# Optimization experiments

Hardware: AMD Instinct MI355X
Metric: run time of the kernel (lower is better)

Reference implementation:

```python
import jax, jax.numpy as jnp
import numpy as np

D = 2048
M = 50000
B = 16384
TOP_K = 5


def setup_inputs() -> dict:
    key = jax.random.key(0)
    ks = jax.random.split(key, 10)
    s = 0.02  # weight init scale
    return {
        "neural_output": jax.random.normal(ks[0], (B, D), dtype=jnp.float32),
        "context_embedding": jax.random.normal(ks[1], (D,), dtype=jnp.float32),
        "memory_bank": jax.random.normal(ks[2], (M, D), dtype=jnp.float32),
        "memory_values": jax.random.normal(ks[3], (M, D), dtype=jnp.float32),
        "Wq": jax.random.normal(ks[4], (D, D), dtype=jnp.float32) * s,
        "bq": jnp.zeros((D,), dtype=jnp.float32),
        "Wk": jax.random.normal(ks[5], (D, D), dtype=jnp.float32) * s,
        "bk": jnp.zeros((D,), dtype=jnp.float32),
        "Wv": jax.random.normal(ks[6], (D, D), dtype=jnp.float32) * s,
        "bv": jnp.zeros((D,), dtype=jnp.float32),
        "Wg": jax.random.normal(ks[7], (D, 2 * D), dtype=jnp.float32) * s,
        "bg": jnp.zeros((D,), dtype=jnp.float32),
        "top_k": TOP_K,
    }


def reference(neural_output, context_embedding, memory_bank, memory_values,
              Wq, bq, Wk, bk, Wv, bv, Wg, bg, top_k):
    d = neural_output.shape[-1]
    eps = 1e-12  # F.normalize eps

    # --- retrieve_memories: cosine similarity + top-k over the full (all-used) bank ---
    q_norm = context_embedding / jnp.maximum(jnp.linalg.norm(context_embedding), eps)
    keys_norm = memory_bank / jnp.maximum(
        jnp.linalg.norm(memory_bank, axis=-1, keepdims=True), eps)
    sims = keys_norm @ q_norm                      # [M]
    top_sims, top_idx = jax.lax.top_k(sims, top_k)  # [K], [K]
    memories = memory_values[top_idx]               # [K, D]

    # --- modulate_neural_activity: tiny cross-attention + gate ---
    q = neural_output @ Wq.T + bq                   # [B, D]
    k = memories @ Wk.T + bk                        # [K, D]
    v = memories @ Wv.T + bv                        # [K, D]
    scores = (q @ k.T) / jnp.sqrt(jnp.float32(d))   # [B, K]
    scores = scores * top_sims[None, :]             # similarity-weighted logits
    attn = jax.nn.softmax(scores, axis=-1)          # [B, K]
    attended = attn @ v                             # [B, D]

    combined = jnp.concatenate([neural_output, attended], axis=-1)  # [B, 2D]
    gate = jax.nn.sigmoid(combined @ Wg.T + bg)     # [B, D]
    return neural_output + gate * attended
```

## Files before the change

### kernel.cpp

```cpp
#include <hip/hip_runtime.h>
#include <hip/hip_bf16.h>
#include <math.h>

#define D 2048
#define M_ROWS 50000
#define B_ROWS 16384
#define TOPK 5
#define EPSN 1e-12f

typedef __attribute__((ext_vector_type(4))) float f32x4;
typedef __attribute__((ext_vector_type(8))) short s16x8;
typedef __attribute__((ext_vector_type(4))) unsigned short u16x4;

__device__ __forceinline__ unsigned short f2bf(float f) {
  union { float f; unsigned int u; } x; x.f = f;
  unsigned int u = x.u;
  unsigned int r = u + 0x7fffu + ((u >> 16) & 1u);
  return (unsigned short)(r >> 16);
}

__device__ __forceinline__ void gload16(const void* g, void* l) {
  __builtin_amdgcn_global_load_lds(
      (const __attribute__((address_space(1))) unsigned int*)g,
      (__attribute__((address_space(3))) unsigned int*)l, 16, 0, 0);
}

__global__ void k_qnorm(const float* __restrict__ ce, float* __restrict__ qn) {
  __shared__ float red[256];
  int tid = threadIdx.x;
  float s = 0.f;
  for (int t = tid; t < D; t += 256) { float x = ce[t]; s += x * x; }
  red[tid] = s; __syncthreads();
  for (int w = 128; w > 0; w >>= 1) { if (tid < w) red[tid] += red[tid + w]; __syncthreads(); }
  float inv = 1.0f / fmaxf(sqrtf(red[0]), EPSN);
  for (int t = tid; t < D; t += 256) qn[t] = ce[t] * inv;
}

__global__ void k_sims(const float* __restrict__ bank, const float* __restrict__ qn,
                       float* __restrict__ sims) {
  __shared__ float qs[D];
  int tid = threadIdx.x;
  for (int t = tid; t < D; t += 256) qs[t] = qn[t];
  __syncthreads();
  int lane = tid & 63, wid = tid >> 6;
  int gw = (blockIdx.x << 2) + wid;
  int nw = gridDim.x << 2;
  for (int m = gw; m < M_ROWS; m += nw) {
    const float* row = bank + (size_t)m * D;
    float dot = 0.f, sq = 0.f;
#pragma unroll
    for (int i = 0; i < 8; ++i) {
      int off = i * 256 + lane * 4;
      f32x4 a = *(const f32x4*)(row + off);
      f32x4 q = *(const f32x4*)(qs + off);
      dot += a[0]*q[0] + a[1]*q[1] + a[2]*q[2] + a[3]*q[3];
      sq  += a[0]*a[0] + a[1]*a[1] + a[2]*a[2] + a[3]*a[3];
    }
    for (int off = 32; off; off >>= 1) {
      dot += __shfl_xor(dot, off, 64);
      sq  += __shfl_xor(sq,  off, 64);
    }
    if (lane == 0) sims[m] = dot / fmaxf(sqrtf(sq), EPSN);
  }
}

__global__ void k_topk(const float* __restrict__ sims, float* __restrict__ top_sims,
                       int* __restrict__ top_idx) {
  __shared__ float sval[256 * TOPK];
  __shared__ int   sidx[256 * TOPK];
  __shared__ float sv2[64 * TOPK];
  __shared__ int   si2[64 * TOPK];
  int tid = threadIdx.x;
  float lv[TOPK]; int li[TOPK];
#pragma unroll
  for (int j = 0; j < TOPK; ++j) { lv[j] = -INFINITY; li[j] = 0x7fffffff; }
  for (int m = tid; m < M_ROWS; m += 256) {
    float v = sims[m];
    if (v > lv[TOPK-1] || (v == lv[TOPK-1] && m < li[TOPK-1])) {
      lv[TOPK-1] = v; li[TOPK-1] = m;
#pragma unroll
      for (int j = TOPK-1; j > 0; --j) {
        bool sw = (lv[j] > lv[j-1]) || (lv[j] == lv[j-1] && li[j] < li[j-1]);
        if (sw) { float tv=lv[j]; lv[j]=lv[j-1]; lv[j-1]=tv; int ti=li[j]; li[j]=li[j-1]; li[j-1]=ti; }
      }
    }
  }
#pragma unroll
  for (int j = 0; j < TOPK; ++j) { sval[tid*TOPK+j] = lv[j]; sidx[tid*TOPK+j] = li[j]; }
  __syncthreads();
  if (tid < 64) {
    float bv[TOPK]; int bi[TOPK];
    for (int j = 0; j < TOPK; ++j) { bv[j] = -INFINITY; bi[j] = 0x7fffffff; }
    for (int c = tid * 20; c < tid * 20 + 20; ++c) {
      float v = sval[c]; int i = sidx[c];
      if (v > bv[TOPK-1] || (v == bv[TOPK-1] && i < bi[TOPK-1])) {
        bv[TOPK-1] = v; bi[TOPK-1] = i;
        for (int j = TOPK-1; j > 0; --j) {
          bool sw = (bv[j] > bv[j-1]) || (bv[j] == bv[j-1] && bi[j] < bi[j-1]);
          if (sw) { float tv=bv[j]; bv[j]=bv[j-1]; bv[j-1]=tv; int ti=bi[j]; bi[j]=bi[j-1]; bi[j-1]=ti; }
        }
      }
    }
    for (int j = 0; j < TOPK; ++j) { sv2[tid*TOPK+j] = bv[j]; si2[tid*TOPK+j] = bi[j]; }
  }
  __syncthreads();
  if (tid == 0) {
    float bvv[TOPK]; int bii[TOPK];
    for (int j = 0; j < TOPK; ++j) { bvv[j] = -INFINITY; bii[j] = 0x7fffffff; }
    for (int c = 0; c < 64 * TOPK; ++c) {
      float v = sv2[c]; int i = si2[c];
      if (v > bvv[TOPK-1] || (v == bvv[TOPK-1] && i < bii[TOPK-1])) {
        bvv[TOPK-1] = v; bii[TOPK-1] = i;
        for (int j = TOPK-1; j > 0; --j) {
          bool sw = (bvv[j] > bvv[j-1]) || (bvv[j] == bvv[j-1] && bii[j] < bii[j-1]);
          if (sw) { float tv=bvv[j]; bvv[j]=bvv[j-1]; bvv[j-1]=tv; int ti=bii[j]; bii[j]=bii[j-1]; bii[j-1]=ti; }
        }
      }
    }
    for (int j = 0; j < TOPK; ++j) { top_sims[j] = bvv[j]; top_idx[j] = bii[j]; }
  }
}

__global__ void k_kv(const float* __restrict__ mvals, const int* __restrict__ top_idx,
                     const float* __restrict__ Wk, const float* __restrict__ bk,
                     const float* __restrict__ Wv, const float* __restrict__ bvp,
                     float* __restrict__ kb, float* __restrict__ vb) {
  __shared__ float mem[TOPK][D];
  int tid = threadIdx.x;
  for (int j = 0; j < TOPK; ++j) {
    const float* src = mvals + (size_t)top_idx[j] * D;
    for (int t = tid; t < D; t += 256) mem[j][t] = src[t];
  }
  __syncthreads();
  int lane = tid & 63, wid = tid >> 6;
  int c = blockIdx.x * 4 + wid;
  const float* wkr = Wk + (size_t)c * D;
  const float* wvr = Wv + (size_t)c * D;
  float ak[TOPK] = {0,0,0,0,0}, av[TOPK] = {0,0,0,0,0};
#pragma unroll 2
  for (int i = 0; i < 8; ++i) {
    int off = i * 256 + lane * 4;
    f32x4 wk4 = *(const f32x4*)(wkr + off);
    f32x4 wv4 = *(const f32x4*)(wvr + off);
#pragma unroll
    for (int j = 0; j < TOPK; ++j) {
      f32x4 mv = *(const f32x4*)(&mem[j][off]);
      ak[j] += mv[0]*wk4[0] + mv[1]*wk4[1] + mv[2]*wk4[2] + mv[3]*wk4[3];
      av[j] += mv[0]*wv4[0] + mv[1]*wv4[1] + mv[2]*wv4[2] + mv[3]*wv4[3];
    }
  }
  for (int off = 32; off; off >>= 1) {
#pragma unroll
    for (int j = 0; j < TOPK; ++j) {
      ak[j] += __shfl_xor(ak[j], off, 64);
      av[j] += __shfl_xor(av[j], off, 64);
    }
  }
  if (lane == 0) {
#pragma unroll
    for (int j = 0; j < TOPK; ++j) { kb[j*D + c] = ak[j] + bk[c]; vb[j*D + c] = av[j] + bvp[c]; }
  }
}

__global__ void k_prep(const float* __restrict__ Wq, const float* __restrict__ bq,
                       const float* __restrict__ Wg,
                       const float* __restrict__ kb, const float* __restrict__ vb,
                       float* __restrict__ KQpart, float* __restrict__ VW,
                       float* __restrict__ sbias, unsigned short* __restrict__ B_sw) {
  __shared__ float sh[TOPK * D];
  int tid = threadIdx.x;
  int bid = blockIdx.x;
  if (bid < 256) {
    int cc = bid >> 3, tc = bid & 7;
    for (int x = tid; x < TOPK * 64; x += 256) sh[x] = kb[(x >> 6) * D + cc * 64 + (x & 63)];
    __syncthreads();
    float acc[TOPK] = {0,0,0,0,0};
    const float* wq = Wq + (size_t)(cc * 64) * D + tc * 256 + tid;
#pragma unroll 4
    for (int c = 0; c < 64; ++c) {
      float w = wq[(size_t)c * D];
#pragma unroll
      for (int j = 0; j < TOPK; ++j) acc[j] += sh[j * 64 + c] * w;
    }
#pragma unroll
    for (int j = 0; j < TOPK; ++j)
      KQpart[(size_t)(cc * TOPK + j) * D + tc * 256 + tid] = acc[j];
  } else if (bid < 768) {
    for (int x = tid; x < TOPK * D; x += 256) sh[x] = vb[x];
    __syncthreads();
    int lane = tid & 63, wid = tid >> 6;
    int c = (bid - 256) * 4 + wid;
    const float* wg = Wg + (size_t)c * (2 * D) + D;
    float acc[TOPK] = {0,0,0,0,0};
#pragma unroll 2
    for (int i = 0; i < 8; ++i) {
      int off = i * 256 + lane * 4;
      f32x4 g4 = *(const f32x4*)(wg + off);
#pragma unroll
      for (int j = 0; j < TOPK; ++j) {
        f32x4 vv = *(const f32x4*)(&sh[j*D + off]);
        acc[j] += vv[0]*g4[0] + vv[1]*g4[1] + vv[2]*g4[2] + vv[3]*g4[3];
      }
    }
    for (int off = 32; off; off >>= 1)
#pragma unroll
      for (int j = 0; j < TOPK; ++j) acc[j] += __shfl_xor(acc[j], off, 64);
    if (lane == 0)
      for (int j = 0; j < TOPK; ++j) VW[j*D + c] = acc[j];
  } else if (bid == 768) {
    for (int j = 0; j < TOPK; ++j) {
      float s = 0.f;
      for (int t = tid; t < D; t += 256) s += bq[t] * kb[j*D + t];
      sh[tid] = s; __syncthreads();
      for (int w = 128; w > 0; w >>= 1) { if (tid < w) sh[tid] += sh[tid + w]; __syncthreads(); }
      if (tid == 0) sbias[j] = sh[0];
      __syncthreads();
    }
  } else {
    int base = (bid - 769) * 1024;
#pragma unroll
    for (int it = 0; it < 4; ++it) {
      int id = base + it * 256 + tid;
      int r = id >> 8;
      int cidx = id & 255;
      int kb_ = cidx >> 3, c = cidx & 7;
      const float* src = Wg + (size_t)r * (2 * D) + kb_ * 64 + c * 8;
      f32x4 a = *(const f32x4*)(src);
      f32x4 b = *(const f32x4*)(src + 4);
      s16x8 p;
      p[0]=(short)f2bf(a[0]); p[1]=(short)f2bf(a[1]); p[2]=(short)f2bf(a[2]); p[3]=(short)f2bf(a[3]);
      p[4]=(short)f2bf(b[0]); p[5]=(short)f2bf(b[1]); p[6]=(short)f2bf(b[2]); p[7]=(short)f2bf(b[3]);
      int dst = kb_ * 64 + ((c ^ (r & 7)) * 8);
      *(s16x8*)(B_sw + (size_t)r * D + dst) = p;
    }
  }
}

__global__ void k_red(const float* __restrict__ KQpart, float* __restrict__ KQ) {
  int x = blockIdx.x * 256 + threadIdx.x;
  float s = 0.f;
#pragma unroll 8
  for (int cc = 0; cc < 32; ++cc) s += KQpart[(size_t)cc * (TOPK * D) + x];
  KQ[x] = s;
}

template <bool WRITE_CAST>
__global__ void k_attn(const float* __restrict__ no, const float* __restrict__ KQ,
                       const float* __restrict__ sbias, const float* __restrict__ top_sims,
                       float* __restrict__ attn, unsigned short* __restrict__ A_sw) {
  __shared__ float kq[TOPK * D];
  int tid = threadIdx.x;
  for (int x = tid; x < TOPK * D; x += 256) kq[x] = KQ[x];
  __syncthreads();
  int lane = tid & 63, wid = tid >> 6;
  int gw = blockIdx.x * 4 + wid, nw = gridDim.x * 4;
  const float inv = 0.02209708691207961f;
  for (int b = gw; b < B_ROWS; b += nw) {
    const float* row = no + (size_t)b * D;
    float acc[TOPK] = {0,0,0,0,0};
    int swz = (b & 7) << 4;
#pragma unroll 2
    for (int i = 0; i < 8; ++i) {
      int off = i * 256 + lane * 4;
      f32x4 n4 = *(const f32x4*)(row + off);
#pragma unroll
      for (int j = 0; j < TOPK; ++j) {
        f32x4 kv = *(const f32x4*)(&kq[j*D + off]);
        acc[j] += n4[0]*kv[0] + n4[1]*kv[1] + n4[2]*kv[2] + n4[3]*kv[3];
      }
      if (WRITE_CAST) {
        u16x4 c4;
        c4[0]=f2bf(n4[0]); c4[1]=f2bf(n4[1]); c4[2]=f2bf(n4[2]); c4[3]=f2bf(n4[3]);
        int bytecol = off * 2;
        *(u16x4*)((char*)A_sw + (size_t)b * (D*2) + (bytecol ^ swz)) = c4;
      }
    }
    for (int off = 32; off; off >>= 1)
#pragma unroll
      for (int j = 0; j < TOPK; ++j) acc[j] += __shfl_xor(acc[j], off, 64);
    if (lane == 0) {
      float s[TOPK], mx = -INFINITY;
      for (int j = 0; j < TOPK; ++j) { s[j] = (acc[j] + sbias[j]) * inv * top_sims[j]; mx = fmaxf(mx, s[j]); }
      float sum = 0.f;
      for (int j = 0; j < TOPK; ++j) { s[j] = __expf(s[j] - mx); sum += s[j]; }
      float r = 1.0f / sum;
      for (int j = 0; j < TOPK; ++j) attn[(size_t)b*TOPK + j] = s[j] * r;
    }
  }
}

union GemmSmem {
  struct { unsigned short A[2][256 * 64]; unsigned short B[2][256 * 64]; } s;
  float ep[4096];
};

__global__ __launch_bounds__(512, 2) void k_gemm_bf(
    const unsigned short* __restrict__ A_sw, const unsigned short* __restrict__ B_sw,
    const float* __restrict__ no, const float* __restrict__ bg,
    const float* __restrict__ attn, const float* __restrict__ vb,
    const float* __restrict__ VW, float* __restrict__ out) {
  __shared__ GemmSmem sm;

  int tid = threadIdx.x;
  int lane = tid & 63, wid = tid >> 6;
  int fr = lane & 15, fg = lane >> 4;
  int wr = wid >> 2, wc = wid & 3;

  int id = blockIdx.x;
  int nt = id & 7, mt = id >> 3;
  int brow = mt * 256, bcol = nt * 256;

  f32x4 acc[8][4];
#pragma unroll
  for (int m = 0; m < 8; ++m)
#pragma unroll
    for (int n = 0; n < 4; ++n) acc[m][n] = (f32x4){0.f, 0.f, 0.f, 0.f};

  const unsigned short* gA[4];
  const unsigned short* gB[4];
  int lofs[4];
#pragma unroll
  for (int i = 0; i < 4; ++i) {
    int cid = i * 512 + tid;
    int row = cid >> 3, cc = cid & 7;
    gA[i] = A_sw + (size_t)(brow + row) * D + cc * 8;
    gB[i] = B_sw + (size_t)(bcol + row) * D + cc * 8;
    lofs[i] = (i * 512 + wid * 64) * 8;
  }

#pragma unroll
  for (int i = 0; i < 4; ++i) {
    gload16(gA[i], sm.s.A[0] + lofs[i]);
    gload16(gB[i], sm.s.B[0] + lofs[i]);
  }
#pragma unroll
  for (int i = 0; i < 4; ++i) { gA[i] += 64; gB[i] += 64; }
  __syncthreads();

  int cur = 0;
  for (int kt = 0; kt < 32; ++kt) {
    if (kt < 31) {
#pragma unroll
      for (int i = 0; i < 4; ++i) {
        gload16(gA[i], sm.s.A[cur ^ 1] + lofs[i]);
        gload16(gB[i], sm.s.B[cur ^ 1] + lofs[i]);
      }
#pragma unroll
      for (int i = 0; i < 4; ++i) { gA[i] += 64; gB[i] += 64; }
    }
    const unsigned short* Ab = sm.s.A[cur];
    const unsigned short* Bb = sm.s.B[cur];
#pragma unroll
    for (int kk = 0; kk < 2; ++kk) {
      s16x8 af[8], bfr[4];
#pragma unroll
      for (int m = 0; m < 8; ++m) {
        int row = wr * 128 + m * 16 + fr;
        int addr = row * 128 + ((kk * 64 + fg * 16) ^ ((row & 7) << 4));
        af[m] = *(const s16x8*)((const char*)Ab + addr);
      }
#pragma unroll
      for (int n = 0; n < 4; ++n) {
        int row = wc * 64 + n * 16 + fr;
        int addr = row * 128 + ((kk * 64 + fg * 16) ^ ((row & 7) << 4));
        bfr[n] = *(const s16x8*)((const char*)Bb + addr);
      }
#pragma unroll
      for (int m = 0; m < 8; ++m)
#pragma unroll
        for (int n = 0; n < 4; ++n)
          acc[m][n] = __builtin_amdgcn_mfma_f32_16x16x32_bf16(af[m], bfr[n], acc[m][n], 0, 0, 0);
    }
    __syncthreads();
    cur ^= 1;
  }

  for (int x = tid; x < 1280; x += 512) sm.ep[x] = attn[(size_t)brow * TOPK + x];
  for (int x = tid; x < 1280; x += 512) { int j = x >> 8, c = x & 255; sm.ep[1280 + x] = VW[j*D + bcol + c]; }
  for (int x = tid; x < 1280; x += 512) { int j = x >> 8, c = x & 255; sm.ep[2560 + x] = vb[j*D + bcol + c]; }
  if (tid < 256) sm.ep[3840 + tid] = bg[bcol + tid];
  __syncthreads();

#pragma unroll
  for (int m = 0; m < 8; ++m) {
    int rbase = wr * 128 + m * 16 + fg * 4;
#pragma unroll
    for (int n = 0; n < 4; ++n) {
      int c = wc * 64 + n * 16 + fr;
      float vw0 = sm.ep[1280 + 0*256 + c], vw1 = sm.ep[1280 + 1*256 + c], vw2 = sm.ep[1280 + 2*256 + c],
            vw3 = sm.ep[1280 + 3*256 + c], vw4 = sm.ep[1280 + 4*256 + c];
      float v0 = sm.ep[2560 + 0*256 + c], v1 = sm.ep[2560 + 1*256 + c], v2 = sm.ep[2560 + 2*256 + c],
            v3 = sm.ep[2560 + 3*256 + c], v4 = sm.ep[2560 + 4*256 + c];
      float bgc = sm.ep[3840 + c];
#pragma unroll
      for (int i = 0; i < 4; ++i) {
        int r = rbase + i;
        float a0 = sm.ep[r*5+0], a1 = sm.ep[r*5+1], a2 = sm.ep[r*5+2], a3 = sm.ep[r*5+3], a4 = sm.ep[r*5+4];
        float gl = acc[m][n][i] + bgc + a0*vw0 + a1*vw1 + a2*vw2 + a3*vw3 + a4*vw4;
        float att = a0*v0 + a1*v1 + a2*v2 + a3*v3 + a4*v4;
        float gate = 1.0f / (1.0f + __expf(-gl));
        size_t gi = (size_t)(brow + r) * D + bcol + c;
        out[gi] = no[gi] + gate * att;
      }
    }
  }
}

#define BM 128
#define BN 128
#define BKf 32
#define LDK (BKf + 8)

__global__ __launch_bounds__(256) void k_gemm_f32(
    const float* __restrict__ no, const float* __restrict__ Wg,
    const float* __restrict__ bg, const float* __restrict__ attn,
    const float* __restrict__ vb, const float* __restrict__ VW,
    float* __restrict__ out) {
  __shared__ unsigned short As[BM * LDK];
  __shared__ unsigned short Bs[BN * LDK];
  __shared__ float ep[2048];

  int tid = threadIdx.x;
  int lane = tid & 63, wid = tid >> 6;
  int brow = blockIdx.x * BM;
  int bcol = blockIdx.y * BN;
  int wr = wid >> 1, wc = wid & 1;

  f32x4 acc[4][4];
#pragma unroll
  for (int m = 0; m < 4; ++m)
#pragma unroll
    for (int n = 0; n < 4; ++n) acc[m][n] = (f32x4){0.f, 0.f, 0.f, 0.f};

  int fr = lane & 15, fg = lane >> 4;

  for (int kt = 0; kt < D / BKf; ++kt) {
    int k0 = kt * BKf;
#pragma unroll
    for (int i = 0; i < 4; ++i) {
      int fid = tid + i * 256;
      int row = fid >> 3, c4 = (fid & 7) * 4;
      f32x4 a4 = *(const f32x4*)(no + (size_t)(brow + row) * D + k0 + c4);
      f32x4 b4 = *(const f32x4*)(Wg + (size_t)(bcol + row) * (2 * D) + k0 + c4);
      u16x4 ab, bb;
      ab[0] = f2bf(a4[0]); ab[1] = f2bf(a4[1]); ab[2] = f2bf(a4[2]); ab[3] = f2bf(a4[3]);
      bb[0] = f2bf(b4[0]); bb[1] = f2bf(b4[1]); bb[2] = f2bf(b4[2]); bb[3] = f2bf(b4[3]);
      *(u16x4*)(&As[row * LDK + c4]) = ab;
      *(u16x4*)(&Bs[row * LDK + c4]) = bb;
    }
    __syncthreads();
    s16x8 af[4], bfr[4];
#pragma unroll
    for (int m = 0; m < 4; ++m) af[m] = *(const s16x8*)(&As[(wr*64 + m*16 + fr) * LDK + fg*8]);
#pragma unroll
    for (int n = 0; n < 4; ++n) bfr[n] = *(const s16x8*)(&Bs[(wc*64 + n*16 + fr) * LDK + fg*8]);
#pragma unroll
    for (int m = 0; m < 4; ++m)
#pragma unroll
      for (int n = 0; n < 4; ++n)
        acc[m][n] = __builtin_amdgcn_mfma_f32_16x16x32_bf16(af[m], bfr[n], acc[m][n], 0, 0, 0);
    __syncthreads();
  }

  for (int x = tid; x < 640; x += 256) ep[x] = attn[(size_t)brow * TOPK + x];
  for (int x = tid; x < 640; x += 256) { int j = x >> 7, c = x & 127; ep[640 + x]  = VW[j*D + bcol + c]; }
  for (int x = tid; x < 640; x += 256) { int j = x >> 7, c = x & 127; ep[1280 + x] = vb[j*D + bcol + c]; }
  if (tid < 128) ep[1920 + tid] = bg[bcol + tid];
  __syncthreads();

#pragma unroll
  for (int m = 0; m < 4; ++m) {
    int rbase = wr * 64 + m * 16 + fg * 4;
#pragma unroll
    for (int n = 0; n < 4; ++n) {
      int c = wc * 64 + n * 16 + fr;
      float vw0 = ep[640 + 0*128 + c], vw1 = ep[640 + 1*128 + c], vw2 = ep[640 + 2*128 + c],
            vw3 = ep[640 + 3*128 + c], vw4 = ep[640 + 4*128 + c];
      float v0 = ep[1280 + 0*128 + c], v1 = ep[1280 + 1*128 + c], v2 = ep[1280 + 2*128 + c],
            v3 = ep[1280 + 3*128 + c], v4 = ep[1280 + 4*128 + c];
      float bgc = ep[1920 + c];
#pragma unroll
      for (int i = 0; i < 4; ++i) {
        int r = rbase + i;
        float a0 = ep[r*5+0], a1 = ep[r*5+1], a2 = ep[r*5+2], a3 = ep[r*5+3], a4 = ep[r*5+4];
        float gl = acc[m][n][i] + bgc + a0*vw0 + a1*vw1 + a2*vw2 + a3*vw3 + a4*vw4;
        float att = a0*v0 + a1*v1 + a2*v2 + a3*v3 + a4*v4;
        float gate = 1.0f / (1.0f + __expf(-gl));
        size_t gi = (size_t)(brow + r) * D + bcol + c;
        out[gi] = no[gi] + gate * att;
      }
    }
  }
}

extern "C" void kernel_launch(void* const* d_in, const int* in_sizes, int n_in,
                              void* d_out, int out_size, void* d_ws, size_t ws_size,
                              hipStream_t stream) {
  (void)in_sizes; (void)n_in; (void)out_size;
  const float* no    = (const float*)d_in[0];
  const float* ce    = (const float*)d_in[1];
  const float* bank  = (const float*)d_in[2];
  const float* mvals = (const float*)d_in[3];
  const float* Wq    = (const float*)d_in[4];
  const float* bq    = (const float*)d_in[5];
  const float* Wk    = (const float*)d_in[6];
  const float* bk    = (const float*)d_in[7];
  const float* Wv    = (const float*)d_in[8];
  const float* bvp   = (const float*)d_in[9];
  const float* Wg    = (const float*)d_in[10];
  const float* bg    = (const float*)d_in[11];
  float* out = (float*)d_out;

  char* ws = (char*)d_ws;
  float* qn       = (float*)(ws + 0);
  float* sims     = (float*)(ws + 16384);
  float* top_sims = (float*)(ws + 220160);
  int*   top_idx  = (int*)  (ws + 220192);
  float* sbias    = (float*)(ws + 220224);
  float* kb       = (float*)(ws + 221184);
  float* vb       = (float*)(ws + 262144);
  float* VW       = (float*)(ws + 303104);
  float* KQpart   = (float*)(ws + 344064);
  float* KQ       = (float*)(ws + 1654784);
  float* attn     = (float*)(ws + 1695744);
  unsigned short* A_sw = (unsigned short*)(ws + 4194304);
  unsigned short* B_sw = (unsigned short*)(ws + 4194304 + (size_t)B_ROWS * D * 2);

  const size_t ws_need = 4194304 + (size_t)B_ROWS * D * 2 + (size_t)D * D * 2;
  const bool fast = ws_size >= ws_need;

  k_qnorm<<<1, 256, 0, stream>>>(ce, qn);
  k_sims<<<1024, 256, 0, stream>>>(bank, qn, sims);
  k_topk<<<1, 256, 0, stream>>>(sims, top_sims, top_idx);
  k_kv<<<512, 256, 0, stream>>>(mvals, top_idx, Wk, bk, Wv, bvp, kb, vb);
  k_prep<<<fast ? 1281 : 769, 256, 0, stream>>>(Wq, bq, Wg, kb, vb, KQpart, VW, sbias, B_sw);
  k_red<<<40, 256, 0, stream>>>(KQpart, KQ);
  if (fast) {
    k_attn<true><<<1024, 256, 0, stream>>>(no, KQ, sbias, top_sims, attn, A_sw);
    k_gemm_bf<<<512, 512, 0, stream>>>(A_sw, B_sw, no, bg, attn, vb, VW, out);
  } else {
    k_attn<false><<<1024, 256, 0, stream>>>(no, KQ, sbias, top_sims, attn, A_sw);
    k_gemm_f32<<<dim3(B_ROWS / BM, D / BN), 256, 0, stream>>>(no, Wg, bg, attn, vb, VW, out);
  }
}
```

Baseline: 562.0 us.

## Pre-tile GEMM operands into MFMA subtiles and interleave loads with MFMA phases

The bf16 cast kernels now write A and B into a 16-row by 64-column subtile layout, so each wave's global-to-LDS copy is one contiguous 1 KB chunk and fragment reads need no XOR swizzle. The GEMM main loop is split into four phases that alternate LDS fragment reads, staging of the next k-tile's halves, and MFMA bursts. These phases use raw s_barrier, explicit waitcnt and setprio so that memory traffic overlaps with compute. Launch bounds drop to one block per SIMD set, which relies on intra-block overlap instead of occupancy and brings a risk of LDS race or stall issues from the hand-tuned waitcnt counts.

```diff
diff --git a/kernel.cpp b/kernel.cpp
--- a/kernel.cpp
+++ b/kernel.cpp
@@ -23,6 +23,11 @@
   __builtin_amdgcn_global_load_lds(
       (const __attribute__((address_space(1))) unsigned int*)g,
       (__attribute__((address_space(3))) unsigned int*)l, 16, 0, 0);
+}
+
+__device__ __forceinline__ size_t sub_addr(int row, int k) {
+  return ((size_t)(row >> 4) * 32 + (size_t)(k >> 6)) * 1024
+       + (size_t)(((k >> 5) & 1) * 512 + ((k >> 3) & 3) * 128 + (row & 15) * 8);
 }
 
 __global__ void k_qnorm(const float* __restrict__ ce, float* __restrict__ qn) {
@@ -220,18 +225,16 @@
     int base = (bid - 769) * 1024;
 #pragma unroll
     for (int it = 0; it < 4; ++it) {
-      int id = base + it * 256 + tid;
-      int r = id >> 8;
-      int cidx = id & 255;
-      int kb_ = cidx >> 3, c = cidx & 7;
-      const float* src = Wg + (size_t)r * (2 * D) + kb_ * 64 + c * 8;
+      int id2 = base + it * 256 + tid;
+      int r = id2 >> 8;
+      int k = (id2 & 255) * 8;
+      const float* src = Wg + (size_t)r * (2 * D) + k;
       f32x4 a = *(const f32x4*)(src);
       f32x4 b = *(const f32x4*)(src + 4);
       s16x8 p;
       p[0]=(short)f2bf(a[0]); p[1]=(short)f2bf(a[1]); p[2]=(short)f2bf(a[2]); p[3]=(short)f2bf(a[3]);
       p[4]=(short)f2bf(b[0]); p[5]=(short)f2bf(b[1]); p[6]=(short)f2bf(b[2]); p[7]=(short)f2bf(b[3]);
-      int dst = kb_ * 64 + ((c ^ (r & 7)) * 8);
-      *(s16x8*)(B_sw + (size_t)r * D + dst) = p;
+      *(s16x8*)(B_sw + sub_addr(r, k)) = p;
     }
   }
 }
@@ -258,21 +261,23 @@
   for (int b = gw; b < B_ROWS; b += nw) {
     const float* row = no + (size_t)b * D;
     float acc[TOPK] = {0,0,0,0,0};
-    int swz = (b & 7) << 4;
-#pragma unroll 2
-    for (int i = 0; i < 8; ++i) {
-      int off = i * 256 + lane * 4;
-      f32x4 n4 = *(const f32x4*)(row + off);
+#pragma unroll
+    for (int i = 0; i < 4; ++i) {
+      int k = i * 512 + lane * 8;
+      f32x4 n4a = *(const f32x4*)(row + k);
+      f32x4 n4b = *(const f32x4*)(row + k + 4);
 #pragma unroll
       for (int j = 0; j < TOPK; ++j) {
-        f32x4 kv = *(const f32x4*)(&kq[j*D + off]);
-        acc[j] += n4[0]*kv[0] + n4[1]*kv[1] + n4[2]*kv[2] + n4[3]*kv[3];
+        f32x4 ka = *(const f32x4*)(&kq[j*D + k]);
+        f32x4 kb2 = *(const f32x4*)(&kq[j*D + k + 4]);
+        acc[j] += n4a[0]*ka[0] + n4a[1]*ka[1] + n4a[2]*ka[2] + n4a[3]*ka[3]
+                + n4b[0]*kb2[0] + n4b[1]*kb2[1] + n4b[2]*kb2[2] + n4b[3]*kb2[3];
       }
       if (WRITE_CAST) {
-        u16x4 c4;
-        c4[0]=f2bf(n4[0]); c4[1]=f2bf(n4[1]); c4[2]=f2bf(n4[2]); c4[3]=f2bf(n4[3]);
-        int bytecol = off * 2;
-        *(u16x4*)((char*)A_sw + (size_t)b * (D*2) + (bytecol ^ swz)) = c4;
+        s16x8 p;
+        p[0]=(short)f2bf(n4a[0]); p[1]=(short)f2bf(n4a[1]); p[2]=(short)f2bf(n4a[2]); p[3]=(short)f2bf(n4a[3]);
+        p[4]=(short)f2bf(n4b[0]); p[5]=(short)f2bf(n4b[1]); p[6]=(short)f2bf(n4b[2]); p[7]=(short)f2bf(n4b[3]);
+        *(s16x8*)(A_sw + sub_addr(b, k)) = p;
       }
     }
     for (int off = 32; off; off >>= 1)
@@ -290,11 +295,18 @@
 }
 
 union GemmSmem {
-  struct { unsigned short A[2][256 * 64]; unsigned short B[2][256 * 64]; } s;
+  struct { unsigned short A[2][16384]; unsigned short B[2][16384]; } s;
   float ep[4096];
 };
 
-__global__ __launch_bounds__(512, 2) void k_gemm_bf(
+#define STAGE(MAT, kt_, kk_, dn_) do {                                          \
+    size_t o0 = (((size_t)(rb##MAT + rh0) * 32 + (size_t)(kt_)) << 10) + ((size_t)(kk_) << 9); \
+    size_t o1 = (((size_t)(rb##MAT + rh1) * 32 + (size_t)(kt_)) << 10) + ((size_t)(kk_) << 9); \
+    gload16(MAT##_sw + o0 + lane * 8, sm.s.MAT[dn_] + rh0 * 1024 + (kk_) * 512); \
+    gload16(MAT##_sw + o1 + lane * 8, sm.s.MAT[dn_] + rh1 * 1024 + (kk_) * 512); \
+  } while (0)
+
+__global__ __launch_bounds__(512, 1) void k_gemm_bf(
     const unsigned short* __restrict__ A_sw, const unsigned short* __restrict__ B_sw,
     const float* __restrict__ no, const float* __restrict__ bg,
     const float* __restrict__ attn, const float* __restrict__ vb,
@@ -305,10 +317,12 @@
   int lane = tid & 63, wid = tid >> 6;
   int fr = lane & 15, fg = lane >> 4;
   int wr = wid >> 2, wc = wid & 3;
+  int rh0 = wid * 2, rh1 = wid * 2 + 1;
 
   int id = blockIdx.x;
   int nt = id & 7, mt = id >> 3;
   int brow = mt * 256, bcol = nt * 256;
+  int rbA = mt * 16, rbB = nt * 16;
 
   f32x4 acc[8][4];
 #pragma unroll
@@ -316,63 +330,85 @@
 #pragma unroll
     for (int n = 0; n < 4; ++n) acc[m][n] = (f32x4){0.f, 0.f, 0.f, 0.f};
 
-  const unsigned short* gA[4];
-  const unsigned short* gB[4];
-  int lofs[4];
-#pragma unroll
-  for (int i = 0; i < 4; ++i) {
-    int cid = i * 512 + tid;
-    int row = cid >> 3, cc = cid & 7;
-    gA[i] = A_sw + (size_t)(brow + row) * D + cc * 8;
-    gB[i] = B_sw + (size_t)(bcol + row) * D + cc * 8;
-    lofs[i] = (i * 512 + wid * 64) * 8;
-  }
-
-#pragma unroll
-  for (int i = 0; i < 4; ++i) {
-    gload16(gA[i], sm.s.A[0] + lofs[i]);
-    gload16(gB[i], sm.s.B[0] + lofs[i]);
-  }
-#pragma unroll
-  for (int i = 0; i < 4; ++i) { gA[i] += 64; gB[i] += 64; }
-  __syncthreads();
-
-  int cur = 0;
+  STAGE(A, 0, 0, 0); STAGE(B, 0, 0, 0);
+  asm volatile("s_waitcnt vmcnt(0)" ::: "memory");
+  STAGE(A, 0, 1, 0); STAGE(B, 0, 1, 0);
+  __builtin_amdgcn_s_barrier();
+
+  s16x8 af[4], bfr[4];
   for (int kt = 0; kt < 32; ++kt) {
-    if (kt < 31) {
-#pragma unroll
-      for (int i = 0; i < 4; ++i) {
-        gload16(gA[i], sm.s.A[cur ^ 1] + lofs[i]);
-        gload16(gB[i], sm.s.B[cur ^ 1] + lofs[i]);
-      }
-#pragma unroll
-      for (int i = 0; i < 4; ++i) { gA[i] += 64; gB[i] += 64; }
-    }
-    const unsigned short* Ab = sm.s.A[cur];
-    const unsigned short* Bb = sm.s.B[cur];
-#pragma unroll
-    for (int kk = 0; kk < 2; ++kk) {
-      s16x8 af[8], bfr[4];
-#pragma unroll
-      for (int m = 0; m < 8; ++m) {
-        int row = wr * 128 + m * 16 + fr;
-        int addr = row * 128 + ((kk * 64 + fg * 16) ^ ((row & 7) << 4));
-        af[m] = *(const s16x8*)((const char*)Ab + addr);
-      }
-#pragma unroll
-      for (int n = 0; n < 4; ++n) {
-        int row = wc * 64 + n * 16 + fr;
-        int addr = row * 128 + ((kk * 64 + fg * 16) ^ ((row & 7) << 4));
-        bfr[n] = *(const s16x8*)((const char*)Bb + addr);
-      }
-#pragma unroll
-      for (int m = 0; m < 8; ++m)
-#pragma unroll
-        for (int n = 0; n < 4; ++n)
-          acc[m][n] = __builtin_amdgcn_mfma_f32_16x16x32_bf16(af[m], bfr[n], acc[m][n], 0, 0, 0);
-    }
-    __syncthreads();
-    cur ^= 1;
+    int d = kt & 1, dn = d ^ 1;
+    const unsigned short* Ab = sm.s.A[d];
+    const unsigned short* Bb = sm.s.B[d];
+    const bool st = (kt < 31);
+    int rdo = fg * 128 + fr * 8;
+
+#pragma unroll
+    for (int m = 0; m < 4; ++m) af[m]  = *(const s16x8*)(Ab + (wr*8 + m)*1024 + rdo);
+#pragma unroll
+    for (int n = 0; n < 4; ++n) bfr[n] = *(const s16x8*)(Bb + (wc*4 + n)*1024 + rdo);
+    if (st) STAGE(A, kt + 1, 0, dn);
+    __builtin_amdgcn_s_barrier();
+    asm volatile("s_waitcnt lgkmcnt(0)" ::: "memory");
+    __builtin_amdgcn_sched_barrier(0);
+    __builtin_amdgcn_s_setprio(1);
+#pragma unroll
+    for (int n = 0; n < 4; ++n)
+#pragma unroll
+      for (int m = 0; m < 4; ++m)
+        acc[m][n] = __builtin_amdgcn_mfma_f32_16x16x32_bf16(af[m], bfr[n], acc[m][n], 0, 0, 0);
+    __builtin_amdgcn_s_setprio(0);
+    __builtin_amdgcn_s_barrier();
+
+#pragma unroll
+    for (int m = 0; m < 4; ++m) af[m] = *(const s16x8*)(Ab + (wr*8 + 4 + m)*1024 + rdo);
+    if (st) STAGE(B, kt + 1, 0, dn);
+    __builtin_amdgcn_s_barrier();
+    asm volatile("s_waitcnt lgkmcnt(0)" ::: "memory");
+    __builtin_amdgcn_sched_barrier(0);
+    __builtin_amdgcn_s_setprio(1);
+#pragma unroll
+    for (int n = 0; n < 4; ++n)
+#pragma unroll
+      for (int m = 0; m < 4; ++m)
+        acc[4 + m][n] = __builtin_amdgcn_mfma_f32_16x16x32_bf16(af[m], bfr[n], acc[4 + m][n], 0, 0, 0);
+    __builtin_amdgcn_s_setprio(0);
+    if (st) asm volatile("s_waitcnt vmcnt(4)" ::: "memory");
+    else    asm volatile("s_waitcnt vmcnt(0)" ::: "memory");
+    __builtin_amdgcn_s_barrier();
+
+#pragma unroll
+    for (int m = 0; m < 4; ++m) af[m]  = *(const s16x8*)(Ab + (wr*8 + m)*1024 + 512 + rdo);
+#pragma unroll
+    for (int n = 0; n < 4; ++n) bfr[n] = *(const s16x8*)(Bb + (wc*4 + n)*1024 + 512 + rdo);
+    if (st) STAGE(A, kt + 1, 1, dn);
+    __builtin_amdgcn_s_barrier();
+    asm volatile("s_waitcnt lgkmcnt(0)" ::: "memory");
+    __builtin_amdgcn_sched_barrier(0);
+    __builtin_amdgcn_s_setprio(1);
+#pragma unroll
+    for (int n = 0; n < 4; ++n)
+#pragma unroll
+      for (int m = 0; m < 4; ++m)
+        acc[m][n] = __builtin_amdgcn_mfma_f32_16x16x32_bf16(af[m], bfr[n], acc[m][n], 0, 0, 0);
+    __builtin_amdgcn_s_setprio(0);
+    __builtin_amdgcn_s_barrier();
+
+#pragma unroll
+    for (int m = 0; m < 4; ++m) af[m] = *(const s16x8*)(Ab + (wr*8 + 4 + m)*1024 + 512 + rdo);
+    if (st) STAGE(B, kt + 1, 1, dn);
+    __builtin_amdgcn_s_barrier();
+    asm volatile("s_waitcnt lgkmcnt(0)" ::: "memory");
+    __builtin_amdgcn_sched_barrier(0);
+    __builtin_amdgcn_s_setprio(1);
+#pragma unroll
+    for (int n = 0; n < 4; ++n)
+#pragma unroll
+      for (int m = 0; m < 4; ++m)
+        acc[4 + m][n] = __builtin_amdgcn_mfma_f32_16x16x32_bf16(af[m], bfr[n], acc[4 + m][n], 0, 0, 0);
+    __builtin_amdgcn_s_setprio(0);
+    if (st) asm volatile("s_waitcnt vmcnt(4)" ::: "memory");
+    __builtin_amdgcn_s_barrier();
   }
 
   for (int x = tid; x < 1280; x += 512) sm.ep[x] = attn[(size_t)brow * TOPK + x];
```

Result: slower. 665.3 us (+18.4%).
